# Optimization experiments

Measured on AMD Instinct MI355X. Metric: run time of the kernel, lower is better.

## Reference

```python
import jax, jax.numpy as jnp
import numpy as np

B, T, DIM = 4, 2048, 256
H, D = 8, 32          # head_num, att_nfths
FFN = 1024
EPS = 1e-5
SLOPE = 0.01          # LeakyReLU default negative slope


def setup_inputs() -> dict:
    key = jax.random.key(0)
    ks = jax.random.split(key, 16)
    s = 0.02
    inp = {
        "x_input": jax.random.normal(ks[0], (B, T, DIM), jnp.float32),
        "x_input_pos": jax.random.normal(ks[1], (B, T, T, H), jnp.float32),
        "padding_matrix": jnp.zeros((B, T, T), jnp.float32),
        "Wq": jax.random.normal(ks[2], (H * D, DIM), jnp.float32) * s,
        "bq": jnp.zeros((H * D,), jnp.float32),
        "Wk": jax.random.normal(ks[3], (H * D, DIM), jnp.float32) * s,
        "bk": jnp.zeros((H * D,), jnp.float32),
        "Wv": jax.random.normal(ks[4], (H * D, DIM), jnp.float32) * s,
        "bv": jnp.zeros((H * D,), jnp.float32),
        "Wo": jax.random.normal(ks[5], (DIM, H * D), jnp.float32) * s,
        "bo": jnp.zeros((DIM,), jnp.float32),
        "W1": jax.random.normal(ks[6], (FFN, DIM), jnp.float32) * s,
        "b1": jnp.zeros((FFN,), jnp.float32),
        "W2": jax.random.normal(ks[7], (DIM, FFN), jnp.float32) * s,
        "b2": jnp.zeros((DIM,), jnp.float32),
        "g1": jnp.ones((DIM,), jnp.float32),
        "be1": jnp.zeros((DIM,), jnp.float32),
        "g2": jnp.ones((DIM,), jnp.float32),
        "be2": jnp.zeros((DIM,), jnp.float32),
    }
    return inp


def _layernorm(x, g, b):
    mu = jnp.mean(x, axis=-1, keepdims=True)
    var = jnp.mean(jnp.square(x - mu), axis=-1, keepdims=True)
    return (x - mu) * jax.lax.rsqrt(var + EPS) * g + b


def reference(x_input, x_input_pos, padding_matrix,
              Wq, bq, Wk, bk, Wv, bv, Wo, bo,
              W1, b1, W2, b2, g1, be1, g2, be2):
    b, t, _ = x_input.shape
    # projections -> (b, t, H, D)
    q = (x_input @ Wq.T + bq).reshape(b, t, H, D)
    k = (x_input @ Wk.T + bk).reshape(b, t, H, D)
    v = (x_input @ Wv.T + bv).reshape(b, t, H, D)
    # scores: (b, H, t, t); note pos bias is added BEFORE the 1/sqrt(D) scaling
    scores = jnp.einsum('bqhd,bkhd->bhqk', q, k)
    scores = (scores + jnp.transpose(x_input_pos, (0, 3, 1, 2))) / np.sqrt(D).astype(np.float32)
    scores = scores + padding_matrix[:, None, :, :]
    att = jax.nn.softmax(scores, axis=-1)
    ctx = jnp.einsum('bhqk,bkhd->bqhd', att, v).reshape(b, t, H * D)
    att_out = ctx @ Wo.T + bo
    x = _layernorm(x_input + att_out, g1, be1)
    h = x @ W1.T + b1
    h = jnp.where(h >= 0, h, SLOPE * h)  # LeakyReLU
    x2 = h @ W2.T + b2
    x = _layernorm(x + x2, g2, be2)
    return x
```

## Files before the change

kernel.cpp:

```cpp
#include <hip/hip_runtime.h>

typedef unsigned short u16;
typedef unsigned int   u32;
typedef float f32x4 __attribute__((ext_vector_type(4)));
typedef u32   u32x4 __attribute__((ext_vector_type(4)));
typedef u16   u16x4 __attribute__((ext_vector_type(4)));
typedef u16   u16x8 __attribute__((ext_vector_type(8)));
typedef __bf16 bf16x8 __attribute__((ext_vector_type(8)));

#define OFF_X    0x0000000ULL
#define OFF_WQ   0x0400000ULL
#define OFF_WO   0x0460000ULL
#define OFF_W1   0x0480000ULL
#define OFF_W2   0x0500000ULL
#define OFF_Q    0x0580000ULL
#define OFF_K    0x0980000ULL
#define OFF_VT   0x0D80000ULL
#define OFF_CTX  0x1180000ULL
#define OFF_X1F  0x1580000ULL
#define OFF_X1B  0x1D80000ULL
#define OFF_H    0x2180000ULL

__device__ __forceinline__ u16 f2bf(float f){
  u32 u = __float_as_uint(f);
  return (u16)((u + 0x7FFFu + ((u >> 16) & 1u)) >> 16);
}
__device__ __forceinline__ u32 cvt_pk(float lo, float hi){
  u32 r;
  asm volatile("v_cvt_pk_bf16_f32 %0, %1, %2" : "=v"(r) : "v"(lo), "v"(hi));
  return r;
}
__device__ __forceinline__ bf16x8 ld_bf8(const u16* p){
  return *(const bf16x8*)p;
}
__device__ __forceinline__ f32x4 ntld4(const float* p){
  return __builtin_nontemporal_load((const f32x4*)p);
}
__device__ __forceinline__ float ntld(const float* p){
  return __builtin_nontemporal_load(p);
}
__device__ __forceinline__ f32x4 MFMA(bf16x8 a, bf16x8 b, f32x4 c){
  return __builtin_amdgcn_mfma_f32_16x16x32_bf16(a, b, c, 0, 0, 0);
}
__device__ __forceinline__ void lbar(){
  asm volatile("s_waitcnt lgkmcnt(0)" ::: "memory");
  __builtin_amdgcn_s_barrier();
}
template<int C>
__device__ __forceinline__ float dpp_rot(float x){
  int i = __float_as_int(x);
  return __int_as_float(__builtin_amdgcn_update_dpp(i, i, C, 0xF, 0xF, false));
}
__device__ __forceinline__ float rmax16(float x){
  x = fmaxf(x, dpp_rot<0x121>(x)); x = fmaxf(x, dpp_rot<0x122>(x));
  x = fmaxf(x, dpp_rot<0x124>(x)); x = fmaxf(x, dpp_rot<0x128>(x));
  return x;
}
__device__ __forceinline__ float rsum16(float x){
  x += dpp_rot<0x121>(x); x += dpp_rot<0x122>(x);
  x += dpp_rot<0x124>(x); x += dpp_rot<0x128>(x);
  return x;
}

__global__ __launch_bounds__(256) void prep_kernel(
    const float* __restrict__ x,  const float* __restrict__ Wq,
    const float* __restrict__ Wk, const float* __restrict__ Wv,
    const float* __restrict__ Wo, const float* __restrict__ W1,
    const float* __restrict__ W2, u16* __restrict__ dst)
{
  int i = (blockIdx.x * 256 + threadIdx.x) * 4;
  const float* src;
  int off;
  if (i < 2097152){ src = x; off = i; }
  else {
    int j = i - 2097152;
    if      (j <  65536){ src = Wq; off = j; }
    else if (j < 131072){ src = Wk; off = j -  65536; }
    else if (j < 196608){ src = Wv; off = j - 131072; }
    else if (j < 262144){ src = Wo; off = j - 196608; }
    else if (j < 524288){ src = W1; off = j - 262144; }
    else                { src = W2; off = j - 524288; }
  }
  f32x4 v = *(const f32x4*)(src + off);
  u16x4 o;
  o[0] = f2bf(v[0]); o[1] = f2bf(v[1]); o[2] = f2bf(v[2]); o[3] = f2bf(v[3]);
  *(u16x4*)(dst + i) = o;
}

__global__ __launch_bounds__(512) void qkv_kernel(
    const u16* __restrict__ X, const u16* __restrict__ W3,
    const float* __restrict__ bq, const float* __restrict__ bk,
    const float* __restrict__ bv,
    u16* __restrict__ Q, u16* __restrict__ K, u16* __restrict__ VT)
{
  __shared__ u16 vtile[32][264];
  const int tid = threadIdx.x;
  const int lane = tid & 63, w = tid >> 6;
  const int g = lane >> 4, c = lane & 15;
  const int m0 = blockIdx.x * 32;
  const int nb = blockIdx.y;
  const u16* Wb = W3 + nb * 65536;
  const float* bias = (nb == 0) ? bq : ((nb == 1) ? bk : bv);
  const int n0 = w * 32;

  f32x4 acc[2][2];
  #pragma unroll
  for (int i = 0; i < 2; ++i)
    #pragma unroll
    for (int j = 0; j < 2; ++j){ f32x4 z = {0.f,0.f,0.f,0.f}; acc[i][j] = z; }

  #pragma unroll
  for (int kt = 0; kt < 8; ++kt){
    bf16x8 a0 = ld_bf8(X  + (size_t)(m0 +      c) * 256 + kt*32 + g*8);
    bf16x8 a1 = ld_bf8(X  + (size_t)(m0 + 16 + c) * 256 + kt*32 + g*8);
    bf16x8 b0 = ld_bf8(Wb + (size_t)(n0 +      c) * 256 + kt*32 + g*8);
    bf16x8 b1 = ld_bf8(Wb + (size_t)(n0 + 16 + c) * 256 + kt*32 + g*8);
    acc[0][0] = MFMA(a0, b0, acc[0][0]);
    acc[0][1] = MFMA(a0, b1, acc[0][1]);
    acc[1][0] = MFMA(a1, b0, acc[1][0]);
    acc[1][1] = MFMA(a1, b1, acc[1][1]);
  }

  const int bi = m0 >> 11, tbase = m0 & 2047;

  if (nb == 2){
    #pragma unroll
    for (int qt = 0; qt < 2; ++qt)
    #pragma unroll
    for (int nt = 0; nt < 2; ++nt)
    #pragma unroll
    for (int r = 0; r < 4; ++r){
      int row = qt*16 + g*4 + r;
      int col = n0 + nt*16 + c;
      vtile[row][col] = f2bf(acc[qt][nt][r] + bias[col]);
    }
    __syncthreads();
    #pragma unroll
    for (int s = 0; s < 2; ++s){
      int u = tid*2 + s;
      int h = u >> 7, d = (u >> 2) & 31, sl0 = (u & 3) * 8;
      u16x8 o;
      #pragma unroll
      for (int jj = 0; jj < 8; ++jj){
        int sl = sl0 + jj;
        int tt = (sl >> 1) + ((sl & 1) << 4);
        o[jj] = vtile[tt][h*32 + d];
      }
      *(u16x8*)(VT + ((size_t)(bi*8 + h) * 32 + d) * 2048 + tbase + sl0) = o;
    }
  } else {
    #pragma unroll
    for (int qt = 0; qt < 2; ++qt)
    #pragma unroll
    for (int nt = 0; nt < 2; ++nt)
    #pragma unroll
    for (int r = 0; r < 4; ++r){
      int mrow = m0 + qt*16 + g*4 + r;
      int col  = n0 + nt*16 + c;
      float v = acc[qt][nt][r] + bias[col];
      int t = mrow & 2047;
      int h = col >> 5, d = col & 31;
      u16 hv = f2bf(v);
      if (nb == 0) Q[((size_t)(bi*8 + h) * 2048 + t) * 32 + d] = hv;
      else         K[((size_t)(bi*8 + h) * 2048 + t) * 32 + d] = hv;
    }
  }
}

__global__ __launch_bounds__(512, 4) void attn_kernel(
    const float* __restrict__ pos, const float* __restrict__ pad,
    const u16* __restrict__ Q, const u16* __restrict__ K,
    const u16* __restrict__ VT, u16* __restrict__ ctx)
{
  __shared__ u32 bias_lds[2][4608];
  __shared__ u32 p_lds[8][16][34];

  const int tid = threadIdx.x;
  const int lane = tid & 63, w = tid >> 6;
  const int g = lane >> 4, c = lane & 15;
  const int bid = blockIdx.x;
  const int xcd = bid & 7;
  const int b = xcd >> 1;
  const int qtile = ((bid >> 3) << 1) | (xcd & 1);
  const int q0 = qtile * 16;

  const u16* Qb  = Q  + ((size_t)(b*8 + w) * 2048 + q0) * 32;
  const u16* Kb  = K  +  (size_t)(b*8 + w) * 2048 * 32;
  const u16* VTb = VT +  (size_t)(b*8 + w) * 32 * 2048;

  const float c1 = 1.4426950408889634f * 0.17677669529663689f;
  const float c2 = 1.4426950408889634f;

  bf16x8 qf = ld_bf8(Qb + (size_t)c * 32 + g*8);

  f32x4 O[2];
  { f32x4 z = {0.f,0.f,0.f,0.f}; O[0] = z; O[1] = z; }
  float m_[4], l_[4];
  #pragma unroll
  for (int r = 0; r < 4; ++r){ m_[r] = -3.0e38f; l_[r] = 0.f; }

  const int li = (lane >> 1) & 15;
  const int ls = lane >> 5;
  const int h0 = (lane & 1) * 4;

  f32x4 fa[2], fb[2];
  float pa_[2], pb_[2];
  bf16x8 kf[4], knf[4], vf[4];

  auto stage_load = [&](int k0){
    #pragma unroll
    for (int j = 0; j < 2; ++j){
      int qr = w*2 + j;
      int k1 = ls*32 + li;
      const float* pr = pos + ((size_t)(b*2048 + q0 + qr) * 2048 + k0) * 8 + h0;
      fa[j] = ntld4(pr + (size_t)k1 * 8);
      fb[j] = ntld4(pr + (size_t)(k1 + 16) * 8);
      const float* dr = pad + (size_t)(b*2048 + q0 + qr) * 2048 + k0 + k1;
      pa_[j] = ntld(dr);
      pb_[j] = ntld(dr + 16);
    }
  };
  auto stage_write = [&](u32* bl){
    #pragma unroll
    for (int j = 0; j < 2; ++j){
      int qr = w*2 + j;
      float plo = pa_[j] * c2, phi = pb_[j] * c2;
      int base = qr*36 + ls*16 + li;
      #pragma unroll
      for (int j2 = 0; j2 < 4; ++j2){
        float lo = fmaf(fa[j][j2], c1, plo);
        float hi = fmaf(fb[j][j2], c1, phi);
        bl[(h0 + j2)*576 + base] = cvt_pk(lo, hi);
      }
    }
  };
  auto load_k = [&](int k0, bf16x8* kd){
    kd[0] = ld_bf8(Kb + (size_t)(k0 +      c) * 32 + g*8);
    kd[1] = ld_bf8(Kb + (size_t)(k0 + 16 + c) * 32 + g*8);
    kd[2] = ld_bf8(Kb + (size_t)(k0 + 32 + c) * 32 + g*8);
    kd[3] = ld_bf8(Kb + (size_t)(k0 + 48 + c) * 32 + g*8);
  };
  auto load_v = [&](int k0){
    vf[0] = ld_bf8(VTb + (size_t)(     c) * 2048 + k0      + g*8);
    vf[1] = ld_bf8(VTb + (size_t)(16 + c) * 2048 + k0      + g*8);
    vf[2] = ld_bf8(VTb + (size_t)(     c) * 2048 + k0 + 32 + g*8);
    vf[3] = ld_bf8(VTb + (size_t)(16 + c) * 2048 + k0 + 32 + g*8);
  };

  stage_load(0);
  stage_write(&bias_lds[0][0]);
  stage_load(64);
  load_k(0, kf);
  lbar();

  for (int t = 0; t < 32; ++t){
    const int k0 = t * 64;
    load_v(k0);
    if (t < 31) stage_write(&bias_lds[(t + 1) & 1][0]);
    if (t < 30) stage_load(k0 + 128);
    if (t < 31) load_k(k0 + 64, knf);

    f32x4 sS[4];
    {
      f32x4 z = {0.f,0.f,0.f,0.f};
      sS[0] = MFMA(qf, kf[0], z);
      sS[1] = MFMA(qf, kf[1], z);
      sS[2] = MFMA(qf, kf[2], z);
      sS[3] = MFMA(qf, kf[3], z);
    }

    const u32* blc = &bias_lds[t & 1][w*576];
    #pragma unroll
    for (int r = 0; r < 4; ++r){
      int rowb = (g*4 + r)*36;
      u32 dwA = blc[rowb + c];
      u32 dwB = blc[rowb + 16 + c];
      float v0 = fmaf(sS[0][r], c1, __uint_as_float(dwA << 16));
      float v1 = fmaf(sS[1][r], c1, __uint_as_float(dwA & 0xFFFF0000u));
      float v2 = fmaf(sS[2][r], c1, __uint_as_float(dwB << 16));
      float v3 = fmaf(sS[3][r], c1, __uint_as_float(dwB & 0xFFFF0000u));
      float mx = rmax16(fmaxf(fmaxf(v0, v1), fmaxf(v2, v3)));
      float mo = m_[r];
      float mn = fmaxf(mo, mx);
      float alpha = exp2f(mo - mn);
      m_[r] = mn;
      float p0 = exp2f(v0 - mn);
      float p1 = exp2f(v1 - mn);
      float p2 = exp2f(v2 - mn);
      float p3 = exp2f(v3 - mn);
      float ps = rsum16((p0 + p1) + (p2 + p3));
      l_[r] = l_[r] * alpha + ps;
      O[0][r] *= alpha;
      O[1][r] *= alpha;
      p_lds[w][g*4 + r][c]      = cvt_pk(p0, p1);
      p_lds[w][g*4 + r][16 + c] = cvt_pk(p2, p3);
    }

    {
      u32x4 t0 = { p_lds[w][c][g*4 + 0], p_lds[w][c][g*4 + 1],
                   p_lds[w][c][g*4 + 2], p_lds[w][c][g*4 + 3] };
      u32x4 t1 = { p_lds[w][c][16 + g*4 + 0], p_lds[w][c][16 + g*4 + 1],
                   p_lds[w][c][16 + g*4 + 2], p_lds[w][c][16 + g*4 + 3] };
      bf16x8 pa0 = __builtin_bit_cast(bf16x8, t0);
      bf16x8 pa1 = __builtin_bit_cast(bf16x8, t1);
      O[0] = MFMA(pa0, vf[0], O[0]);
      O[1] = MFMA(pa0, vf[1], O[1]);
      O[0] = MFMA(pa1, vf[2], O[0]);
      O[1] = MFMA(pa1, vf[3], O[1]);
    }

    #pragma unroll
    for (int i = 0; i < 4; ++i) kf[i] = knf[i];
    lbar();
  }

  #pragma unroll
  for (int r = 0; r < 4; ++r){
    float inv = 1.0f / l_[r];
    int q = q0 + g*4 + r;
    size_t base = (size_t)(b*2048 + q) * 256 + w*32;
    ctx[base +      c] = f2bf(O[0][r] * inv);
    ctx[base + 16 + c] = f2bf(O[1][r] * inv);
  }
}

template<int KSTEPS>
__global__ __launch_bounds__(512) void gemm_ln_kernel(
    const u16* __restrict__ A, const u16* __restrict__ Wt,
    const float* __restrict__ bias, const float* __restrict__ resid,
    const float* __restrict__ gam, const float* __restrict__ bet,
    float* __restrict__ outF, u16* __restrict__ outB, int lda)
{
  __shared__ float sm1[32][8], sm2[32][8];
  const int tid = threadIdx.x;
  const int lane = tid & 63, w = tid >> 6;
  const int g = lane >> 4, c = lane & 15;
  const int m0 = blockIdx.x * 32;
  const int n0 = w * 32;

  const u16* Am = A  + (size_t)m0 * lda;
  const u16* Wn = Wt + (size_t)n0 * lda;

  f32x4 acc[2][2];
  #pragma unroll
  for (int i = 0; i < 2; ++i)
    #pragma unroll
    for (int j = 0; j < 2; ++j){ f32x4 z = {0.f,0.f,0.f,0.f}; acc[i][j] = z; }

  #pragma unroll 4
  for (int kt = 0; kt < KSTEPS; ++kt){
    bf16x8 a0 = ld_bf8(Am + (size_t)(     c) * lda + kt*32 + g*8);
    bf16x8 a1 = ld_bf8(Am + (size_t)(16 + c) * lda + kt*32 + g*8);
    bf16x8 b0 = ld_bf8(Wn + (size_t)(     c) * lda + kt*32 + g*8);
    bf16x8 b1 = ld_bf8(Wn + (size_t)(16 + c) * lda + kt*32 + g*8);
    acc[0][0] = MFMA(a0, b0, acc[0][0]);
    acc[0][1] = MFMA(a0, b1, acc[0][1]);
    acc[1][0] = MFMA(a1, b0, acc[1][0]);
    acc[1][1] = MFMA(a1, b1, acc[1][1]);
  }

  float val[2][2][4];
  #pragma unroll
  for (int qt = 0; qt < 2; ++qt)
  #pragma unroll
  for (int nt = 0; nt < 2; ++nt)
  #pragma unroll
  for (int r = 0; r < 4; ++r){
    int mrow = m0 + qt*16 + g*4 + r;
    int col  = n0 + nt*16 + c;
    val[qt][nt][r] = acc[qt][nt][r] + bias[col] + resid[(size_t)mrow*256 + col];
  }

  #pragma unroll
  for (int qt = 0; qt < 2; ++qt)
  #pragma unroll
  for (int r = 0; r < 4; ++r){
    float v0 = val[qt][0][r], v1 = val[qt][1][r];
    float p1 = rsum16(v0 + v1);
    float p2 = rsum16(v0*v0 + v1*v1);
    if (c == 0){
      int rr = qt*16 + g*4 + r;
      sm1[rr][w] = p1; sm2[rr][w] = p2;
    }
  }
  __syncthreads();

  #pragma unroll
  for (int qt = 0; qt < 2; ++qt)
  #pragma unroll
  for (int r = 0; r < 4; ++r){
    int rr = qt*16 + g*4 + r;
    float S1 = 0.f, S2 = 0.f;
    #pragma unroll
    for (int j = 0; j < 8; ++j){ S1 += sm1[rr][j]; S2 += sm2[rr][j]; }
    float mean = S1 * (1.0f/256.0f);
    float var  = S2 * (1.0f/256.0f) - mean*mean;
    float rstd = rsqrtf(var + 1e-5f);
    int mrow = m0 + rr;
    #pragma unroll
    for (int nt = 0; nt < 2; ++nt){
      int col = n0 + nt*16 + c;
      float y = (val[qt][nt][r] - mean) * rstd * gam[col] + bet[col];
      outF[(size_t)mrow*256 + col] = y;
      if (outB) outB[(size_t)mrow*256 + col] = f2bf(y);
    }
  }
}

__global__ __launch_bounds__(512) void ffn1_kernel(
    const u16* __restrict__ X1, const u16* __restrict__ W1b,
    const float* __restrict__ b1, u16* __restrict__ Hb)
{
  const int tid = threadIdx.x;
  const int lane = tid & 63, w = tid >> 6;
  const int g = lane >> 4, c = lane & 15;
  const int m0 = blockIdx.x * 32;
  const int n0 = blockIdx.y * 256 + w * 32;

  const u16* Am = X1  + (size_t)m0 * 256;
  const u16* Wn = W1b + (size_t)n0 * 256;

  f32x4 acc[2][2];
  #pragma unroll
  for (int i = 0; i < 2; ++i)
    #pragma unroll
    for (int j = 0; j < 2; ++j){ f32x4 z = {0.f,0.f,0.f,0.f}; acc[i][j] = z; }

  #pragma unroll
  for (int kt = 0; kt < 8; ++kt){
    bf16x8 a0 = ld_bf8(Am + (size_t)(     c) * 256 + kt*32 + g*8);
    bf16x8 a1 = ld_bf8(Am + (size_t)(16 + c) * 256 + kt*32 + g*8);
    bf16x8 b0 = ld_bf8(Wn + (size_t)(     c) * 256 + kt*32 + g*8);
    bf16x8 b1 = ld_bf8(Wn + (size_t)(16 + c) * 256 + kt*32 + g*8);
    acc[0][0] = MFMA(a0, b0, acc[0][0]);
    acc[0][1] = MFMA(a0, b1, acc[0][1]);
    acc[1][0] = MFMA(a1, b0, acc[1][0]);
    acc[1][1] = MFMA(a1, b1, acc[1][1]);
  }

  #pragma unroll
  for (int qt = 0; qt < 2; ++qt)
  #pragma unroll
  for (int nt = 0; nt < 2; ++nt)
  #pragma unroll
  for (int r = 0; r < 4; ++r){
    int mrow = m0 + qt*16 + g*4 + r;
    int col  = n0 + nt*16 + c;
    float v = acc[qt][nt][r] + b1[col];
    v = (v >= 0.f) ? v : v * 0.01f;
    Hb[(size_t)mrow*1024 + col] = f2bf(v);
  }
}

extern "C" void kernel_launch(void* const* d_in, const int* in_sizes, int n_in,
                              void* d_out, int out_size, void* d_ws, size_t ws_size,
                              hipStream_t stream)
{
  (void)in_sizes; (void)n_in; (void)out_size; (void)ws_size;
  const float* x   = (const float*)d_in[0];
  const float* pos = (const float*)d_in[1];
  const float* pad = (const float*)d_in[2];
  const float* Wq  = (const float*)d_in[3];
  const float* bq  = (const float*)d_in[4];
  const float* Wk  = (const float*)d_in[5];
  const float* bk  = (const float*)d_in[6];
  const float* Wv  = (const float*)d_in[7];
  const float* bv  = (const float*)d_in[8];
  const float* Wo  = (const float*)d_in[9];
  const float* bo  = (const float*)d_in[10];
  const float* W1  = (const float*)d_in[11];
  const float* b1  = (const float*)d_in[12];
  const float* W2  = (const float*)d_in[13];
  const float* b2  = (const float*)d_in[14];
  const float* g1  = (const float*)d_in[15];
  const float* be1 = (const float*)d_in[16];
  const float* g2  = (const float*)d_in[17];
  const float* be2 = (const float*)d_in[18];

  char* ws = (char*)d_ws;
  u16* wsX  = (u16*)(ws + OFF_X);
  u16* wsW3 = (u16*)(ws + OFF_WQ);
  u16* wsWo = (u16*)(ws + OFF_WO);
  u16* wsW1 = (u16*)(ws + OFF_W1);
  u16* wsW2 = (u16*)(ws + OFF_W2);
  u16* Qb   = (u16*)(ws + OFF_Q);
  u16* Kb   = (u16*)(ws + OFF_K);
  u16* VTb  = (u16*)(ws + OFF_VT);
  u16* ctx  = (u16*)(ws + OFF_CTX);
  float* x1f = (float*)(ws + OFF_X1F);
  u16* x1b  = (u16*)(ws + OFF_X1B);
  u16* hb   = (u16*)(ws + OFF_H);

  prep_kernel<<<2816, 256, 0, stream>>>(x, Wq, Wk, Wv, Wo, W1, W2, wsX);
  qkv_kernel<<<dim3(256, 3), 512, 0, stream>>>(wsX, wsW3, bq, bk, bv, Qb, Kb, VTb);
  attn_kernel<<<512, 512, 0, stream>>>(pos, pad, Qb, Kb, VTb, ctx);
  gemm_ln_kernel<8><<<256, 512, 0, stream>>>(ctx, wsWo, bo, x, g1, be1, x1f, x1b, 256);
  ffn1_kernel<<<dim3(256, 4), 512, 0, stream>>>(x1b, wsW1, b1, hb);
  gemm_ln_kernel<32><<<256, 512, 0, stream>>>(hb, wsW2, b2, x1f, g2, be2,
                                              (float*)d_out, (u16*)nullptr, 1024);
}
```

Measured before the change: 278.6 us.

## Fuse output projection, LayerNorm, FFN and second LayerNorm into one tail kernel

Replaces the three tail kernels (Wo GEMM+LN1, FFN1, FFN2+LN2) with a single kernel per 32-row tile. The LN1 output and the FFN hidden activations stay in swizzled LDS instead of going through global memory, and the hidden dimension is processed in two halves of 512. This removes two launches and the global round-trips of x1 (fp32 and bf16) and of the 8 MB hidden tensor. In exchange, the whole tail runs on only 256 blocks, and each block streams all of W1 and W2 serially, which lowers parallelism and adds more barriers.

```diff
diff --git a/kernel.cpp b/kernel.cpp
--- a/kernel.cpp
+++ b/kernel.cpp
@@ -17,9 +17,6 @@
 #define OFF_K    0x0980000ULL
 #define OFF_VT   0x0D80000ULL
 #define OFF_CTX  0x1180000ULL
-#define OFF_X1F  0x1580000ULL
-#define OFF_X1B  0x1D80000ULL
-#define OFF_H    0x2180000ULL
 
 __device__ __forceinline__ u16 f2bf(float f){
   u32 u = __float_as_uint(f);
@@ -31,6 +28,9 @@
   return r;
 }
 __device__ __forceinline__ bf16x8 ld_bf8(const u16* p){
+  return *(const bf16x8*)p;
+}
+__device__ __forceinline__ bf16x8 lds_bf8(const u16* p){
   return *(const bf16x8*)p;
 }
 __device__ __forceinline__ f32x4 ntld4(const float* p){
@@ -324,39 +324,41 @@
   }
 }
 
-template<int KSTEPS>
-__global__ __launch_bounds__(512) void gemm_ln_kernel(
-    const u16* __restrict__ A, const u16* __restrict__ Wt,
-    const float* __restrict__ bias, const float* __restrict__ resid,
-    const float* __restrict__ gam, const float* __restrict__ bet,
-    float* __restrict__ outF, u16* __restrict__ outB, int lda)
+__global__ __launch_bounds__(512, 2) void tail_kernel(
+    const u16* __restrict__ ctx, const u16* __restrict__ Wo,
+    const float* __restrict__ bo, const float* __restrict__ x,
+    const float* __restrict__ g1, const float* __restrict__ be1,
+    const u16* __restrict__ W1, const float* __restrict__ b1,
+    const u16* __restrict__ W2, const float* __restrict__ b2,
+    const float* __restrict__ g2, const float* __restrict__ be2,
+    float* __restrict__ out)
 {
+  __shared__ u16 x1t[32*256];
+  __shared__ u16 ht[32*512];
   __shared__ float sm1[32][8], sm2[32][8];
+
   const int tid = threadIdx.x;
   const int lane = tid & 63, w = tid >> 6;
   const int g = lane >> 4, c = lane & 15;
   const int m0 = blockIdx.x * 32;
   const int n0 = w * 32;
 
-  const u16* Am = A  + (size_t)m0 * lda;
-  const u16* Wn = Wt + (size_t)n0 * lda;
-
   f32x4 acc[2][2];
   #pragma unroll
   for (int i = 0; i < 2; ++i)
     #pragma unroll
     for (int j = 0; j < 2; ++j){ f32x4 z = {0.f,0.f,0.f,0.f}; acc[i][j] = z; }
 
-  #pragma unroll 4
-  for (int kt = 0; kt < KSTEPS; ++kt){
-    bf16x8 a0 = ld_bf8(Am + (size_t)(     c) * lda + kt*32 + g*8);
-    bf16x8 a1 = ld_bf8(Am + (size_t)(16 + c) * lda + kt*32 + g*8);
-    bf16x8 b0 = ld_bf8(Wn + (size_t)(     c) * lda + kt*32 + g*8);
-    bf16x8 b1 = ld_bf8(Wn + (size_t)(16 + c) * lda + kt*32 + g*8);
+  #pragma unroll
+  for (int kt = 0; kt < 8; ++kt){
+    bf16x8 a0 = ld_bf8(ctx + (size_t)(m0 +      c) * 256 + kt*32 + g*8);
+    bf16x8 a1 = ld_bf8(ctx + (size_t)(m0 + 16 + c) * 256 + kt*32 + g*8);
+    bf16x8 b0 = ld_bf8(Wo  + (size_t)(n0 +      c) * 256 + kt*32 + g*8);
+    bf16x8 b1v= ld_bf8(Wo  + (size_t)(n0 + 16 + c) * 256 + kt*32 + g*8);
     acc[0][0] = MFMA(a0, b0, acc[0][0]);
-    acc[0][1] = MFMA(a0, b1, acc[0][1]);
+    acc[0][1] = MFMA(a0, b1v, acc[0][1]);
     acc[1][0] = MFMA(a1, b0, acc[1][0]);
-    acc[1][1] = MFMA(a1, b1, acc[1][1]);
+    acc[1][1] = MFMA(a1, b1v, acc[1][1]);
   }
 
   float val[2][2][4];
@@ -368,7 +370,7 @@
   for (int r = 0; r < 4; ++r){
     int mrow = m0 + qt*16 + g*4 + r;
     int col  = n0 + nt*16 + c;
-    val[qt][nt][r] = acc[qt][nt][r] + bias[col] + resid[(size_t)mrow*256 + col];
+    val[qt][nt][r] = acc[qt][nt][r] + bo[col] + x[(size_t)mrow*256 + col];
   }
 
   #pragma unroll
@@ -385,6 +387,116 @@
   }
   __syncthreads();
 
+  float yv[2][2][4];
+  #pragma unroll
+  for (int qt = 0; qt < 2; ++qt)
+  #pragma unroll
+  for (int r = 0; r < 4; ++r){
+    int rr = qt*16 + g*4 + r;
+    float S1 = 0.f, S2 = 0.f;
+    #pragma unroll
+    for (int j = 0; j < 8; ++j){ S1 += sm1[rr][j]; S2 += sm2[rr][j]; }
+    float mean = S1 * (1.0f/256.0f);
+    float var  = S2 * (1.0f/256.0f) - mean*mean;
+    float rstd = rsqrtf(var + 1e-5f);
+    #pragma unroll
+    for (int nt = 0; nt < 2; ++nt){
+      int col = n0 + nt*16 + c;
+      float y = (val[qt][nt][r] - mean) * rstd * g1[col] + be1[col];
+      yv[qt][nt][r] = y;
+      int elem = rr*256 + col;
+      x1t[elem ^ ((rr & 7) << 3)] = f2bf(y);
+    }
+  }
+  __syncthreads();
+
+  f32x4 acc3[2][2];
+  #pragma unroll
+  for (int i = 0; i < 2; ++i)
+    #pragma unroll
+    for (int j = 0; j < 2; ++j){ f32x4 z = {0.f,0.f,0.f,0.f}; acc3[i][j] = z; }
+
+  #pragma unroll
+  for (int half = 0; half < 2; ++half){
+    #pragma unroll
+    for (int ns = 0; ns < 2; ++ns){
+      const int ncol = half*512 + w*64 + ns*32;
+      f32x4 acc2[2][2];
+      #pragma unroll
+      for (int i = 0; i < 2; ++i)
+        #pragma unroll
+        for (int j = 0; j < 2; ++j){ f32x4 z = {0.f,0.f,0.f,0.f}; acc2[i][j] = z; }
+      #pragma unroll
+      for (int kt = 0; kt < 8; ++kt){
+        int e0 = (     c)*256 + kt*32 + g*8;
+        int e1 = (16 + c)*256 + kt*32 + g*8;
+        bf16x8 a0 = lds_bf8(x1t + (e0 ^ ((c & 7) << 3)));
+        bf16x8 a1 = lds_bf8(x1t + (e1 ^ (((16 + c) & 7) << 3)));
+        bf16x8 b0 = ld_bf8(W1 + (size_t)(ncol +      c) * 256 + kt*32 + g*8);
+        bf16x8 b1v= ld_bf8(W1 + (size_t)(ncol + 16 + c) * 256 + kt*32 + g*8);
+        acc2[0][0] = MFMA(a0, b0, acc2[0][0]);
+        acc2[0][1] = MFMA(a0, b1v, acc2[0][1]);
+        acc2[1][0] = MFMA(a1, b0, acc2[1][0]);
+        acc2[1][1] = MFMA(a1, b1v, acc2[1][1]);
+      }
+      #pragma unroll
+      for (int qt = 0; qt < 2; ++qt)
+      #pragma unroll
+      for (int nt = 0; nt < 2; ++nt)
+      #pragma unroll
+      for (int r = 0; r < 4; ++r){
+        int row = qt*16 + g*4 + r;
+        int gcol = ncol + nt*16 + c;
+        float v = acc2[qt][nt][r] + b1[gcol];
+        v = (v >= 0.f) ? v : v * 0.01f;
+        int elem = row*512 + (gcol - half*512);
+        ht[elem ^ ((row & 7) << 3)] = f2bf(v);
+      }
+    }
+    __syncthreads();
+
+    #pragma unroll
+    for (int kt = 0; kt < 16; ++kt){
+      int e0 = (     c)*512 + kt*32 + g*8;
+      int e1 = (16 + c)*512 + kt*32 + g*8;
+      bf16x8 a0 = lds_bf8(ht + (e0 ^ ((c & 7) << 3)));
+      bf16x8 a1 = lds_bf8(ht + (e1 ^ (((16 + c) & 7) << 3)));
+      int kg = half*512 + kt*32 + g*8;
+      bf16x8 b0 = ld_bf8(W2 + (size_t)(n0 +      c) * 1024 + kg);
+      bf16x8 b1v= ld_bf8(W2 + (size_t)(n0 + 16 + c) * 1024 + kg);
+      acc3[0][0] = MFMA(a0, b0, acc3[0][0]);
+      acc3[0][1] = MFMA(a0, b1v, acc3[0][1]);
+      acc3[1][0] = MFMA(a1, b0, acc3[1][0]);
+      acc3[1][1] = MFMA(a1, b1v, acc3[1][1]);
+    }
+    __syncthreads();
+  }
+
+  float val3[2][2][4];
+  #pragma unroll
+  for (int qt = 0; qt < 2; ++qt)
+  #pragma unroll
+  for (int nt = 0; nt < 2; ++nt)
+  #pragma unroll
+  for (int r = 0; r < 4; ++r){
+    int col = n0 + nt*16 + c;
+    val3[qt][nt][r] = acc3[qt][nt][r] + b2[col] + yv[qt][nt][r];
+  }
+
+  #pragma unroll
+  for (int qt = 0; qt < 2; ++qt)
+  #pragma unroll
+  for (int r = 0; r < 4; ++r){
+    float v0 = val3[qt][0][r], v1 = val3[qt][1][r];
+    float p1 = rsum16(v0 + v1);
+    float p2 = rsum16(v0*v0 + v1*v1);
+    if (c == 0){
+      int rr = qt*16 + g*4 + r;
+      sm1[rr][w] = p1; sm2[rr][w] = p2;
+    }
+  }
+  __syncthreads();
+
   #pragma unroll
   for (int qt = 0; qt < 2; ++qt)
   #pragma unroll
@@ -400,55 +512,8 @@
     #pragma unroll
     for (int nt = 0; nt < 2; ++nt){
       int col = n0 + nt*16 + c;
-      float y = (val[qt][nt][r] - mean) * rstd * gam[col] + bet[col];
-      outF[(size_t)mrow*256 + col] = y;
-      if (outB) outB[(size_t)mrow*256 + col] = f2bf(y);
-    }
-  }
-}
-
-__global__ __launch_bounds__(512) void ffn1_kernel(
-    const u16* __restrict__ X1, const u16* __restrict__ W1b,
-    const float* __restrict__ b1, u16* __restrict__ Hb)
-{
-  const int tid = threadIdx.x;
-  const int lane = tid & 63, w = tid >> 6;
-  const int g = lane >> 4, c = lane & 15;
-  const int m0 = blockIdx.x * 32;
-  const int n0 = blockIdx.y * 256 + w * 32;
-
-  const u16* Am = X1  + (size_t)m0 * 256;
-  const u16* Wn = W1b + (size_t)n0 * 256;
-
-  f32x4 acc[2][2];
-  #pragma unroll
-  for (int i = 0; i < 2; ++i)
-    #pragma unroll
-    for (int j = 0; j < 2; ++j){ f32x4 z = {0.f,0.f,0.f,0.f}; acc[i][j] = z; }
-
-  #pragma unroll
-  for (int kt = 0; kt < 8; ++kt){
-    bf16x8 a0 = ld_bf8(Am + (size_t)(     c) * 256 + kt*32 + g*8);
-    bf16x8 a1 = ld_bf8(Am + (size_t)(16 + c) * 256 + kt*32 + g*8);
-    bf16x8 b0 = ld_bf8(Wn + (size_t)(     c) * 256 + kt*32 + g*8);
-    bf16x8 b1 = ld_bf8(Wn + (size_t)(16 + c) * 256 + kt*32 + g*8);
-    acc[0][0] = MFMA(a0, b0, acc[0][0]);
-    acc[0][1] = MFMA(a0, b1, acc[0][1]);
-    acc[1][0] = MFMA(a1, b0, acc[1][0]);
-    acc[1][1] = MFMA(a1, b1, acc[1][1]);
-  }
-
-  #pragma unroll
-  for (int qt = 0; qt < 2; ++qt)
-  #pragma unroll
-  for (int nt = 0; nt < 2; ++nt)
-  #pragma unroll
-  for (int r = 0; r < 4; ++r){
-    int mrow = m0 + qt*16 + g*4 + r;
-    int col  = n0 + nt*16 + c;
-    float v = acc[qt][nt][r] + b1[col];
-    v = (v >= 0.f) ? v : v * 0.01f;
-    Hb[(size_t)mrow*1024 + col] = f2bf(v);
+      out[(size_t)mrow*256 + col] = (val3[qt][nt][r] - mean) * rstd * g2[col] + be2[col];
+    }
   }
 }
 
@@ -487,15 +552,10 @@
   u16* Kb   = (u16*)(ws + OFF_K);
   u16* VTb  = (u16*)(ws + OFF_VT);
   u16* ctx  = (u16*)(ws + OFF_CTX);
-  float* x1f = (float*)(ws + OFF_X1F);
-  u16* x1b  = (u16*)(ws + OFF_X1B);
-  u16* hb   = (u16*)(ws + OFF_H);
 
   prep_kernel<<<2816, 256, 0, stream>>>(x, Wq, Wk, Wv, Wo, W1, W2, wsX);
   qkv_kernel<<<dim3(256, 3), 512, 0, stream>>>(wsX, wsW3, bq, bk, bv, Qb, Kb, VTb);
   attn_kernel<<<512, 512, 0, stream>>>(pos, pad, Qb, Kb, VTb, ctx);
-  gemm_ln_kernel<8><<<256, 512, 0, stream>>>(ctx, wsWo, bo, x, g1, be1, x1f, x1b, 256);
-  ffn1_kernel<<<dim3(256, 4), 512, 0, stream>>>(x1b, wsW1, b1, hb);
-  gemm_ln_kernel<32><<<256, 512, 0, stream>>>(hb, wsW2, b2, x1f, g2, be2,
-                                              (float*)d_out, (u16*)nullptr, 1024);
-}
+  tail_kernel<<<256, 512, 0, stream>>>(ctx, wsWo, bo, x, g1, be1,
+                                       wsW1, b1, wsW2, b2, g2, be2, (float*)d_out);
+}
```

Measured after the change: 243.8 us. 12.5% less time.
